# Optimization experiments

Measured on AMD Instinct MI355X. Metric: run time of the kernel, lower is better.

Reference implementation:

```python
import jax, jax.numpy as jnp
import numpy as np

N_NODES = 50000
N_EDGES = 1600000
IN_DIM = 128
OUT_DIM = 16
N_HEADS = 8


def setup_inputs() -> dict:
    key = jax.random.key(0)
    ks = jax.random.split(key, 9)
    s = 1.0 / np.sqrt(IN_DIM)
    return {
        "h": jax.random.normal(ks[0], (N_NODES, IN_DIM), jnp.float32),
        "Wq": jax.random.normal(ks[1], (IN_DIM, OUT_DIM * N_HEADS), jnp.float32) * s,
        "bq": jax.random.normal(ks[2], (OUT_DIM * N_HEADS,), jnp.float32) * 0.01,
        "Wk": jax.random.normal(ks[3], (IN_DIM, OUT_DIM * N_HEADS), jnp.float32) * s,
        "bk": jax.random.normal(ks[4], (OUT_DIM * N_HEADS,), jnp.float32) * 0.01,
        "Wv": jax.random.normal(ks[5], (IN_DIM, OUT_DIM * N_HEADS), jnp.float32) * s,
        "bv": jax.random.normal(ks[6], (OUT_DIM * N_HEADS,), jnp.float32) * 0.01,
        "src": jax.random.randint(ks[7], (N_EDGES,), 0, N_NODES, jnp.int32),
        "dst": jax.random.randint(ks[8], (N_EDGES,), 0, N_NODES, jnp.int32),
    }


def reference(h, Wq, bq, Wk, bk, Wv, bv, src, dst):
    n_nodes = h.shape[0]
    # node-wise Q/K/V projections -> [N, H, D]
    Q = (h @ Wq + bq).reshape(n_nodes, N_HEADS, OUT_DIM)
    K = (h @ Wk + bk).reshape(n_nodes, N_HEADS, OUT_DIM)
    V = (h @ Wv + bv).reshape(n_nodes, N_HEADS, OUT_DIM)
    # edge-wise score: (K[src] * Q[dst]).sum(-1), scaled-exp with clamp
    score = jnp.sum(K[src] * Q[dst], axis=-1)  # [E, H]
    score = jnp.exp(jnp.clip(score / np.sqrt(OUT_DIM), -5.0, 5.0))
    # scatter-sum weighted values and normalizers to dst nodes
    msg = V[src] * score[:, :, None]  # [E, H, D]
    wV = jax.ops.segment_sum(msg, dst, num_segments=n_nodes)  # [N, H, D]
    z = jax.ops.segment_sum(score, dst, num_segments=n_nodes)  # [N, H]
    return wV / (z[:, :, None] + 1e-6)
```

## Files before the change

### kernel.cpp

```cpp
#include <hip/hip_runtime.h>
#include <hip/hip_bf16.h>
#include <cstddef>

#define N_NODES 50000
#define N_EDGES 1600000
#define IN_DIM 128
#define OUT_DIM 16
#define N_HEADS 8
#define QKV_DIM 128
#define HS_STRIDE 136
#define OS_STRIDE 392

#define SUBB 3125
#define BCAP 1024
#define BH_CHUNK 8192
#define BH_BLOCKS 196
#define GEMM_BLOCKS 782
#define FUSED_BLOCKS (BH_BLOCKS + GEMM_BLOCKS)

typedef __hip_bfloat16 bf16;
typedef short bf16x8 __attribute__((ext_vector_type(8)));
typedef float f32x4  __attribute__((ext_vector_type(4)));

__device__ __forceinline__ float b2f(bf16 x) { return __bfloat162float(x); }

__device__ __forceinline__ float u16tof(unsigned int u) {
    unsigned int x = u << 16;
    float f;
    __builtin_memcpy(&f, &x, 4);
    return f;
}

__device__ __forceinline__ unsigned short f2bf(float v) {
    bf16 b = __float2bfloat16(v);
    unsigned short u;
    __builtin_memcpy(&u, &b, 2);
    return u;
}

__global__ __launch_bounds__(256) void sentinel_kernel(unsigned short* __restrict__ out, int n) {
    int i = blockIdx.x * 256 + threadIdx.x;
    if (i < n) out[i] = 0x42C8;
}

__global__ __launch_bounds__(256) void prep_kernel(
    const unsigned short* __restrict__ hraw,
    const void* __restrict__ Wqr, const void* __restrict__ bqr,
    const void* __restrict__ Wkr, const void* __restrict__ bkr,
    const void* __restrict__ Wvr, const void* __restrict__ bvr,
    int* __restrict__ flag,
    unsigned short* __restrict__ Wfrag, float* __restrict__ bias_f)
{
    __shared__ int red[256];
    const int t   = threadIdx.x;
    const int tid = blockIdx.x * 256 + t;

    int cnt = 0;
    for (int i = t; i < 8192; i += 256) {
        unsigned short u = hraw[i];
        int e = (u >> 7) & 0xFF;
        if (e == 0xFF || e > 0x85 || (e == 0 && (u & 0x7F) != 0)) cnt++;
    }
    red[t] = cnt;
    __syncthreads();
    for (int s = 128; s > 0; s >>= 1) {
        if (t < s) red[t] += red[t + s];
        __syncthreads();
    }
    const bool f32 = (red[0] > 100);
    if (blockIdx.x == 0 && t == 0) *flag = red[0];

    if (tid < 384) {
        int mat = tid >> 7, c = tid & 127;
        const void* bp = (mat == 0) ? bqr : (mat == 1) ? bkr : bvr;
        bias_f[tid] = f32 ? ((const float*)bp)[c] : b2f(((const bf16*)bp)[c]);
    }

    int l  = tid & 63;
    int s  = (tid >> 6) & 3;
    int nt = tid >> 8;
    int n  = nt * 16 + (l & 15);
    int k0 = s * 32 + (l >> 4) * 8;
    int mat = n >> 7, c = n & 127;
    const void* Wp = (mat == 0) ? Wqr : (mat == 1) ? Wkr : Wvr;

    unsigned short v[8];
#pragma unroll
    for (int j = 0; j < 8; ++j) {
        int k = k0 + j;
        float w = f32 ? ((const float*)Wp)[k * QKV_DIM + c]
                      : b2f(((const bf16*)Wp)[k * QKV_DIM + c]);
        v[j] = f2bf(w);
    }
    ushort4* o = (ushort4*)(Wfrag + (size_t)tid * 8);
    o[0] = make_ushort4(v[0], v[1], v[2], v[3]);
    o[1] = make_ushort4(v[4], v[5], v[6], v[7]);
}

__global__ __launch_bounds__(256) void fused_gs_kernel(
    const void* __restrict__ hraw,
    const unsigned short* __restrict__ Wfrag, const float* __restrict__ bias_f,
    const int* __restrict__ flag,
    unsigned short* __restrict__ Qt, unsigned short* __restrict__ KVt,
    const int* __restrict__ src, const int* __restrict__ dst,
    unsigned int* __restrict__ packed, unsigned int* __restrict__ offcnt)
{
    __shared__ __align__(16) unsigned char arena[64 * OS_STRIDE * 2];
    const int t = threadIdx.x;

    if (blockIdx.x < BH_BLOCKS) {
        int* lcnt           = (int*)arena;
        unsigned int* stage = (unsigned int*)(arena + 12544);
        int* sm             = (int*)(arena + 45312);
        int* carryp         = (int*)(arena + 46336);

        const int b    = blockIdx.x;
        const int base = b * BH_CHUNK;
        const int nb   = min(N_EDGES - base, BH_CHUNK);

        for (int i = t; i < SUBB; i += 256) lcnt[i] = 0;
        if (t == 0) *carryp = 0;
        __syncthreads();

        for (int i = t; i < nb; i += 256)
            atomicAdd(&lcnt[dst[base + i] >> 4], 1);
        __syncthreads();

        for (int c = 0; c < 13; ++c) {
            int i = c * 256 + t;
            int x = (i < SUBB) ? lcnt[i] : 0;
            int v = x;
            sm[t] = v;
            __syncthreads();
            for (int s = 1; s < 256; s <<= 1) {
                int a = (t >= s) ? sm[t - s] : 0;
                __syncthreads();
                v += a;
                sm[t] = v;
                __syncthreads();
            }
            int off = *carryp + v - x;
            if (i < SUBB) {
                offcnt[(size_t)b * SUBB + i] =
                    ((unsigned int)off << 16) | (unsigned int)x;
                lcnt[i] = off;
            }
            __syncthreads();
            if (t == 255) *carryp += v;
            __syncthreads();
        }

        for (int i = t; i < nb; i += 256) {
            int d = dst[base + i];
            int bk = d >> 4;
            int pos = atomicAdd(&lcnt[bk], 1);
            stage[pos] = (unsigned int)src[base + i] | ((unsigned int)(d & 15) << 16);
        }
        __syncthreads();

        for (int i = t; i < nb; i += 256)
            packed[base + i] = stage[i];

    } else {
        unsigned short* smem = (unsigned short*)arena;

        const bool f32 = (*flag > 100);
        const int m0 = (blockIdx.x - BH_BLOCKS) * 64;

#pragma unroll
        for (int it = 0; it < 8; ++it) {
            int idx = it * 1024 + t * 4;
            int r = idx >> 7, k = idx & 127;
            int row = m0 + r;
            ushort4 w4 = make_ushort4(0, 0, 0, 0);
            if (row < N_NODES) {
                if (f32) {
                    float4 v4 = ((const float4*)hraw)[(size_t)row * 32 + (k >> 2)];
                    w4 = make_ushort4(f2bf(v4.x), f2bf(v4.y), f2bf(v4.z), f2bf(v4.w));
                } else {
                    uint2 u = ((const uint2*)hraw)[(size_t)row * 32 + (k >> 2)];
                    w4 = make_ushort4((unsigned short)(u.x & 0xffffu), (unsigned short)(u.x >> 16),
                                      (unsigned short)(u.y & 0xffffu), (unsigned short)(u.y >> 16));
                }
            }
            *(ushort4*)&smem[r * HS_STRIDE + k] = w4;
        }
        __syncthreads();

        const int lane = t & 63;
        const int wave = t >> 6;
        const int qd   = lane >> 4;
        const int ln15 = lane & 15;

        bf16x8 afr[4][4];
#pragma unroll
        for (int ms = 0; ms < 4; ++ms)
#pragma unroll
            for (int s = 0; s < 4; ++s)
                afr[ms][s] = *(const bf16x8*)&smem[(ms * 16 + ln15) * HS_STRIDE + s * 32 + qd * 8];

        __syncthreads();

#pragma unroll
        for (int i = 0; i < 6; ++i) {
            const int nt  = wave + i * 4;
            const int col = nt * 16 + ln15;
            const float bs = bias_f[col];
            const int mat = col >> 7, c127 = col & 127;
            const int ocol = (mat == 0) ? c127
                           : 128 + 8 * (c127 >> 2) + (c127 & 3) + ((mat == 2) ? 4 : 0);

            bf16x8 bfr[4];
#pragma unroll
            for (int s = 0; s < 4; ++s)
                bfr[s] = *(const bf16x8*)(Wfrag + ((size_t)(nt * 4 + s) * 64 + lane) * 8);

#pragma unroll
            for (int ms = 0; ms < 4; ++ms) {
                f32x4 acc = {0.f, 0.f, 0.f, 0.f};
#pragma unroll
                for (int s = 0; s < 4; ++s)
                    acc = __builtin_amdgcn_mfma_f32_16x16x32_bf16(afr[ms][s], bfr[s], acc, 0, 0, 0);
#pragma unroll
                for (int r = 0; r < 4; ++r) {
                    int rl = ms * 16 + qd * 4 + r;
                    smem[rl * OS_STRIDE + ocol] = f2bf(acc[r] + bs);
                }
            }
        }
        __syncthreads();

        for (int q = t; q < 1024; q += 256) {
            int row = q >> 4, c = q & 15;
            int grow = m0 + row;
            if (grow < N_NODES)
                ((uint4*)Qt)[grow * 16 + c] = *(const uint4*)&smem[row * OS_STRIDE + c * 8];
        }
        for (int q = t; q < 2048; q += 256) {
            int row = q >> 5, g = q & 31;
            int grow = m0 + row;
            if (grow < N_NODES)
                ((uint4*)KVt)[grow * 32 + g] = *(const uint4*)&smem[row * OS_STRIDE + 128 + g * 8];
        }
    }
}

__global__ __launch_bounds__(256) void bucket_agg_kernel(
    const unsigned short* __restrict__ Qt, const unsigned short* __restrict__ KVt,
    const unsigned int* __restrict__ packed, const unsigned int* __restrict__ offcnt,
    const int* __restrict__ flag, void* __restrict__ out)
{
    __shared__ unsigned int   lds_pk[BCAP];
    __shared__ unsigned short lds_src[BCAP];
    __shared__ int runoff[BH_BLOCKS], runcnt[BH_BLOCKS], runpfx[BH_BLOCKS];
    __shared__ int cnt16[16], base16[16], cur16[16];
    __shared__ int nb_s;

    const int sb = blockIdx.x;
    const int t  = threadIdx.x;

    if (t < 16) { cnt16[t] = 0; cur16[t] = 0; }
    if (t < BH_BLOCKS) {
        unsigned int oc = offcnt[(size_t)t * SUBB + sb];
        runoff[t] = t * BH_CHUNK + (int)(oc >> 16);
        runcnt[t] = (int)(oc & 0xffffu);
    }
    __syncthreads();

    {
        int* sm = (int*)lds_pk;
        int x = (t < BH_BLOCKS) ? runcnt[t] : 0;
        int v = x;
        sm[t] = v;
        __syncthreads();
        for (int s = 1; s < 256; s <<= 1) {
            int a = (t >= s) ? sm[t - s] : 0;
            __syncthreads();
            v += a;
            sm[t] = v;
            __syncthreads();
        }
        if (t < BH_BLOCKS) runpfx[t] = v - x;
        if (t == 255) nb_s = v;
        __syncthreads();
    }
    const int nb = min(nb_s, BCAP);

    for (int r = t; r < BH_BLOCKS; r += 256) {
        int ro = runoff[r], rc = runcnt[r], rp = runpfx[r];
        for (int j = 0; j < rc; ++j) {
            int dpos = rp + j;
            if (dpos < BCAP) {
                unsigned int pk = packed[ro + j];
                lds_pk[dpos] = pk;
                atomicAdd(&cnt16[(pk >> 16) & 15], 1);
            }
        }
    }
    __syncthreads();
    if (t == 0) {
        int acc = 0;
#pragma unroll
        for (int i = 0; i < 16; ++i) { base16[i] = acc; acc += cnt16[i]; }
    }
    __syncthreads();
    for (int j = t; j < nb; j += 256) {
        unsigned int pk = lds_pk[j];
        int dl = (pk >> 16) & 15;
        int pos = base16[dl] + atomicAdd(&cur16[dl], 1);
        lds_src[pos] = (unsigned short)(pk & 0xffffu);
    }
    __syncthreads();

    const int wave = t >> 6;
    const int lane = t & 63;
    const int half = lane >> 5;
    const int hl   = lane & 31;
    const uint4* KV4 = (const uint4*)KVt;
    const bool of32 = (*flag > 100);

    for (int dl = wave; dl < 16; dl += 4) {
        const int d = sb * 16 + dl;
        uint2 qw = ((const uint2*)Qt)[d * 32 + hl];
        const float q0 = u16tof(qw.x & 0xffffu), q1 = u16tof(qw.x >> 16);
        const float q2 = u16tof(qw.y & 0xffffu), q3 = u16tof(qw.y >> 16);
        const int off = base16[dl];
        const int n   = cnt16[dl];

        float a0 = 0.f, a1 = 0.f, a2 = 0.f, a3 = 0.f, zz = 0.f;

#define CONSUME(KV, SCMASK)                                                     \
        {                                                                       \
            float p = fmaf(u16tof((KV).x & 0xffffu), q0,                        \
                      fmaf(u16tof((KV).x >> 16), q1,                            \
                      fmaf(u16tof((KV).y & 0xffffu), q2,                        \
                           u16tof((KV).y >> 16) * q3)));                        \
            p += __shfl_xor(p, 1);                                              \
            p += __shfl_xor(p, 2);                                              \
            float sc = __expf(__builtin_amdgcn_fmed3f(p * 0.25f, -5.f, 5.f));   \
            sc *= (SCMASK);                                                     \
            a0 = fmaf(u16tof((KV).z & 0xffffu), sc, a0);                        \
            a1 = fmaf(u16tof((KV).z >> 16),     sc, a1);                        \
            a2 = fmaf(u16tof((KV).w & 0xffffu), sc, a2);                        \
            a3 = fmaf(u16tof((KV).w >> 16),     sc, a3);                        \
            zz += sc;                                                           \
        }

        int j = 0;
        for (; j + 8 <= n; j += 8) {
            int e[4];
#pragma unroll
            for (int u = 0; u < 4; ++u) e[u] = lds_src[off + j + 2 * u + half];
            uint4 kv[4];
#pragma unroll
            for (int u = 0; u < 4; ++u) kv[u] = KV4[e[u] * 32 + hl];
#pragma unroll
            for (int u = 0; u < 4; ++u) CONSUME(kv[u], 1.f)
        }
        for (; j + 2 <= n; j += 2) {
            int e = lds_src[off + j + half];
            uint4 kv = KV4[e * 32 + hl];
            CONSUME(kv, 1.f)
        }
        if (j < n) {
            int e = lds_src[off + j];
            uint4 kv = KV4[e * 32 + hl];
            CONSUME(kv, (half == 0) ? 1.f : 0.f)
        }
#undef CONSUME

        a0 += __shfl_xor(a0, 32);
        a1 += __shfl_xor(a1, 32);
        a2 += __shfl_xor(a2, 32);
        a3 += __shfl_xor(a3, 32);
        zz += __shfl_xor(zz, 32);

        const float inv = 1.f / (zz + 1e-6f);
        const float r0 = a0 * inv, r1 = a1 * inv, r2 = a2 * inv, r3 = a3 * inv;

        if (half == 0) {
            if (of32) {
                ((float4*)out)[d * 32 + hl] = make_float4(r0, r1, r2, r3);
            } else {
                unsigned int w0 = ((unsigned int)f2bf(r1) << 16) | f2bf(r0);
                unsigned int w1 = ((unsigned int)f2bf(r3) << 16) | f2bf(r2);
                ((uint2*)out)[d * 32 + hl] = make_uint2(w0, w1);
            }
        }
    }
}

extern "C" void kernel_launch(void* const* d_in, const int* in_sizes, int n_in,
                              void* d_out, int out_size, void* d_ws, size_t ws_size,
                              hipStream_t stream)
{
    const void* h  = d_in[0];
    const void* Wq = d_in[1];
    const void* bq = d_in[2];
    const void* Wk = d_in[3];
    const void* bk = d_in[4];
    const void* Wv = d_in[5];
    const void* bv = d_in[6];
    const int*  src = (const int*)d_in[7];
    const int*  dst = (const int*)d_in[8];

    const size_t NQ = (size_t)N_NODES * QKV_DIM;
    const size_t WFRAG_N = 24 * 4 * 64 * 8;
    const size_t PACKED_N = (size_t)BH_BLOCKS * BH_CHUNK;
    const size_t OFFCNT_N = (size_t)BH_BLOCKS * SUBB;

    const size_t need = 3 * NQ * 2 + WFRAG_N * 2 + 384 * 4 + 64
                      + PACKED_N * 4 + OFFCNT_N * 4;

    if (ws_size < need) {
        sentinel_kernel<<<(out_size + 255) / 256, 256, 0, stream>>>((unsigned short*)d_out, out_size);
        return;
    }

    unsigned short* Qt  = (unsigned short*)d_ws;
    unsigned short* KVt = Qt + NQ;
    unsigned short* Wfrag = KVt + 2 * NQ;
    float* bias_f = (float*)(Wfrag + WFRAG_N);
    int* flag     = (int*)(bias_f + 384);
    unsigned int* packed = (unsigned int*)(flag + 16);
    unsigned int* offcnt = packed + PACKED_N;

    prep_kernel<<<24, 256, 0, stream>>>((const unsigned short*)h,
        Wq, bq, Wk, bk, Wv, bv, flag, Wfrag, bias_f);

    fused_gs_kernel<<<FUSED_BLOCKS, 256, 0, stream>>>(h, Wfrag, bias_f, flag,
        Qt, KVt, src, dst, packed, offcnt);

    bucket_agg_kernel<<<SUBB, 256, 0, stream>>>(Qt, KVt, packed, offcnt, flag, d_out);
}
```

Before: 256.1 us.

## Scatter edges into fixed-capacity global buckets and shrink GEMM tile to 32 rows

Replaces the per-block prefix-scan and offset/count table with global per-bucket atomic cursors, so edges are written directly into fixed-capacity (768) slots per 16-node bucket. The aggregation kernel then reads one contiguous run per bucket instead of gathering 196 runs. The GEMM part now uses 32-row tiles with a smaller LDS arena and writes Q, K and V in three passes, which should raise occupancy. The risk is that bucket slots are silently truncated when a bucket holds more than GCAP edges, and the atomic cursor ordering is nondeterministic.

```diff
diff --git a/kernel.cpp b/kernel.cpp
--- a/kernel.cpp
+++ b/kernel.cpp
@@ -9,13 +9,13 @@
 #define N_HEADS 8
 #define QKV_DIM 128
 #define HS_STRIDE 136
-#define OS_STRIDE 392
 
 #define SUBB 3125
-#define BCAP 1024
+#define GCAP 768
 #define BH_CHUNK 8192
 #define BH_BLOCKS 196
-#define GEMM_BLOCKS 782
+#define GEMM_M 32
+#define GEMM_BLOCKS 1563
 #define FUSED_BLOCKS (BH_BLOCKS + GEMM_BLOCKS)
 
 typedef __hip_bfloat16 bf16;
@@ -49,11 +49,14 @@
     const void* __restrict__ Wkr, const void* __restrict__ bkr,
     const void* __restrict__ Wvr, const void* __restrict__ bvr,
     int* __restrict__ flag,
-    unsigned short* __restrict__ Wfrag, float* __restrict__ bias_f)
+    unsigned short* __restrict__ Wfrag, float* __restrict__ bias_f,
+    int* __restrict__ gcur)
 {
     __shared__ int red[256];
     const int t   = threadIdx.x;
     const int tid = blockIdx.x * 256 + t;
+
+    for (int i = tid; i < SUBB; i += 24 * 256) gcur[i] = 0;
 
     int cnt = 0;
     for (int i = t; i < 8192; i += 256) {
@@ -103,72 +106,47 @@
     const int* __restrict__ flag,
     unsigned short* __restrict__ Qt, unsigned short* __restrict__ KVt,
     const int* __restrict__ src, const int* __restrict__ dst,
-    unsigned int* __restrict__ packed, unsigned int* __restrict__ offcnt)
+    unsigned int* __restrict__ gpacked, int* __restrict__ gcur)
 {
-    __shared__ __align__(16) unsigned char arena[64 * OS_STRIDE * 2];
+    __shared__ __align__(16) unsigned char arena[12544];
     const int t = threadIdx.x;
 
     if (blockIdx.x < BH_BLOCKS) {
-        int* lcnt           = (int*)arena;
-        unsigned int* stage = (unsigned int*)(arena + 12544);
-        int* sm             = (int*)(arena + 45312);
-        int* carryp         = (int*)(arena + 46336);
+        int* lcnt = (int*)arena;
 
         const int b    = blockIdx.x;
         const int base = b * BH_CHUNK;
         const int nb   = min(N_EDGES - base, BH_CHUNK);
 
         for (int i = t; i < SUBB; i += 256) lcnt[i] = 0;
-        if (t == 0) *carryp = 0;
         __syncthreads();
 
         for (int i = t; i < nb; i += 256)
             atomicAdd(&lcnt[dst[base + i] >> 4], 1);
         __syncthreads();
 
-        for (int c = 0; c < 13; ++c) {
-            int i = c * 256 + t;
-            int x = (i < SUBB) ? lcnt[i] : 0;
-            int v = x;
-            sm[t] = v;
-            __syncthreads();
-            for (int s = 1; s < 256; s <<= 1) {
-                int a = (t >= s) ? sm[t - s] : 0;
-                __syncthreads();
-                v += a;
-                sm[t] = v;
-                __syncthreads();
-            }
-            int off = *carryp + v - x;
-            if (i < SUBB) {
-                offcnt[(size_t)b * SUBB + i] =
-                    ((unsigned int)off << 16) | (unsigned int)x;
-                lcnt[i] = off;
-            }
-            __syncthreads();
-            if (t == 255) *carryp += v;
-            __syncthreads();
-        }
+        for (int i = t; i < SUBB; i += 256) {
+            int c = lcnt[i];
+            if (c) lcnt[i] = i * GCAP + atomicAdd(&gcur[i], c);
+        }
+        __syncthreads();
 
         for (int i = t; i < nb; i += 256) {
-            int d = dst[base + i];
+            int d  = dst[base + i];
             int bk = d >> 4;
             int pos = atomicAdd(&lcnt[bk], 1);
-            stage[pos] = (unsigned int)src[base + i] | ((unsigned int)(d & 15) << 16);
-        }
-        __syncthreads();
-
-        for (int i = t; i < nb; i += 256)
-            packed[base + i] = stage[i];
+            if (pos < (bk + 1) * GCAP)
+                gpacked[pos] = (unsigned int)src[base + i] | ((unsigned int)(d & 15) << 16);
+        }
 
     } else {
         unsigned short* smem = (unsigned short*)arena;
 
         const bool f32 = (*flag > 100);
-        const int m0 = (blockIdx.x - BH_BLOCKS) * 64;
-
-#pragma unroll
-        for (int it = 0; it < 8; ++it) {
+        const int m0 = (blockIdx.x - BH_BLOCKS) * GEMM_M;
+
+#pragma unroll
+        for (int it = 0; it < 4; ++it) {
             int idx = it * 1024 + t * 4;
             int r = idx >> 7, k = idx & 127;
             int row = m0 + r;
@@ -192,9 +170,9 @@
         const int qd   = lane >> 4;
         const int ln15 = lane & 15;
 
-        bf16x8 afr[4][4];
-#pragma unroll
-        for (int ms = 0; ms < 4; ++ms)
+        bf16x8 afr[2][4];
+#pragma unroll
+        for (int ms = 0; ms < 2; ++ms)
 #pragma unroll
             for (int s = 0; s < 4; ++s)
                 afr[ms][s] = *(const bf16x8*)&smem[(ms * 16 + ln15) * HS_STRIDE + s * 32 + qd * 8];
@@ -202,100 +180,78 @@
         __syncthreads();
 
 #pragma unroll
-        for (int i = 0; i < 6; ++i) {
-            const int nt  = wave + i * 4;
-            const int col = nt * 16 + ln15;
-            const float bs = bias_f[col];
-            const int mat = col >> 7, c127 = col & 127;
-            const int ocol = (mat == 0) ? c127
-                           : 128 + 8 * (c127 >> 2) + (c127 & 3) + ((mat == 2) ? 4 : 0);
-
-            bf16x8 bfr[4];
-#pragma unroll
-            for (int s = 0; s < 4; ++s)
-                bfr[s] = *(const bf16x8*)(Wfrag + ((size_t)(nt * 4 + s) * 64 + lane) * 8);
-
-#pragma unroll
-            for (int ms = 0; ms < 4; ++ms) {
-                f32x4 acc = {0.f, 0.f, 0.f, 0.f};
+        for (int p = 0; p < 3; ++p) {
+#pragma unroll
+            for (int ii = 0; ii < 2; ++ii) {
+                const int i   = 2 * p + ii;
+                const int nt  = wave + i * 4;
+                const int col = nt * 16 + ln15;
+                const float bs = bias_f[col];
+                const int c127 = col & 127;
+
+                bf16x8 bfr[4];
 #pragma unroll
                 for (int s = 0; s < 4; ++s)
-                    acc = __builtin_amdgcn_mfma_f32_16x16x32_bf16(afr[ms][s], bfr[s], acc, 0, 0, 0);
-#pragma unroll
-                for (int r = 0; r < 4; ++r) {
-                    int rl = ms * 16 + qd * 4 + r;
-                    smem[rl * OS_STRIDE + ocol] = f2bf(acc[r] + bs);
+                    bfr[s] = *(const bf16x8*)(Wfrag + ((size_t)(nt * 4 + s) * 64 + lane) * 8);
+
+#pragma unroll
+                for (int ms = 0; ms < 2; ++ms) {
+                    f32x4 acc = {0.f, 0.f, 0.f, 0.f};
+#pragma unroll
+                    for (int s = 0; s < 4; ++s)
+                        acc = __builtin_amdgcn_mfma_f32_16x16x32_bf16(afr[ms][s], bfr[s], acc, 0, 0, 0);
+#pragma unroll
+                    for (int r = 0; r < 4; ++r) {
+                        int rl = ms * 16 + qd * 4 + r;
+                        smem[rl * HS_STRIDE + c127] = f2bf(acc[r] + bs);
+                    }
                 }
             }
-        }
-        __syncthreads();
-
-        for (int q = t; q < 1024; q += 256) {
-            int row = q >> 4, c = q & 15;
-            int grow = m0 + row;
-            if (grow < N_NODES)
-                ((uint4*)Qt)[grow * 16 + c] = *(const uint4*)&smem[row * OS_STRIDE + c * 8];
-        }
-        for (int q = t; q < 2048; q += 256) {
-            int row = q >> 5, g = q & 31;
-            int grow = m0 + row;
-            if (grow < N_NODES)
-                ((uint4*)KVt)[grow * 32 + g] = *(const uint4*)&smem[row * OS_STRIDE + 128 + g * 8];
+            __syncthreads();
+            if (p == 0) {
+                for (int q = t; q < 512; q += 256) {
+                    int row = q >> 4, c = q & 15;
+                    int grow = m0 + row;
+                    if (grow < N_NODES)
+                        ((uint4*)Qt)[grow * 16 + c] = *(const uint4*)&smem[row * HS_STRIDE + c * 8];
+                }
+            } else {
+                for (int q = t; q < 1024; q += 256) {
+                    int row = q >> 5, g = q & 31;
+                    int grow = m0 + row;
+                    if (grow < N_NODES)
+                        ((uint2*)KVt)[(size_t)grow * 64 + g * 2 + (p - 1)] =
+                            *(const uint2*)&smem[row * HS_STRIDE + g * 4];
+                }
+            }
+            __syncthreads();
         }
     }
 }
 
 __global__ __launch_bounds__(256) void bucket_agg_kernel(
     const unsigned short* __restrict__ Qt, const unsigned short* __restrict__ KVt,
-    const unsigned int* __restrict__ packed, const unsigned int* __restrict__ offcnt,
+    const unsigned int* __restrict__ gpacked, const int* __restrict__ gcur,
     const int* __restrict__ flag, void* __restrict__ out)
 {
-    __shared__ unsigned int   lds_pk[BCAP];
-    __shared__ unsigned short lds_src[BCAP];
-    __shared__ int runoff[BH_BLOCKS], runcnt[BH_BLOCKS], runpfx[BH_BLOCKS];
+    __shared__ unsigned int   lds_pk[GCAP];
+    __shared__ unsigned short lds_src[GCAP];
     __shared__ int cnt16[16], base16[16], cur16[16];
-    __shared__ int nb_s;
+    __shared__ int n_s;
 
     const int sb = blockIdx.x;
     const int t  = threadIdx.x;
 
     if (t < 16) { cnt16[t] = 0; cur16[t] = 0; }
-    if (t < BH_BLOCKS) {
-        unsigned int oc = offcnt[(size_t)t * SUBB + sb];
-        runoff[t] = t * BH_CHUNK + (int)(oc >> 16);
-        runcnt[t] = (int)(oc & 0xffffu);
-    }
-    __syncthreads();
-
-    {
-        int* sm = (int*)lds_pk;
-        int x = (t < BH_BLOCKS) ? runcnt[t] : 0;
-        int v = x;
-        sm[t] = v;
-        __syncthreads();
-        for (int s = 1; s < 256; s <<= 1) {
-            int a = (t >= s) ? sm[t - s] : 0;
-            __syncthreads();
-            v += a;
-            sm[t] = v;
-            __syncthreads();
-        }
-        if (t < BH_BLOCKS) runpfx[t] = v - x;
-        if (t == 255) nb_s = v;
-        __syncthreads();
-    }
-    const int nb = min(nb_s, BCAP);
-
-    for (int r = t; r < BH_BLOCKS; r += 256) {
-        int ro = runoff[r], rc = runcnt[r], rp = runpfx[r];
-        for (int j = 0; j < rc; ++j) {
-            int dpos = rp + j;
-            if (dpos < BCAP) {
-                unsigned int pk = packed[ro + j];
-                lds_pk[dpos] = pk;
-                atomicAdd(&cnt16[(pk >> 16) & 15], 1);
-            }
-        }
+    if (t == 0) n_s = min(gcur[sb], GCAP);
+    __syncthreads();
+    const int n  = n_s;
+    const int gb = sb * GCAP;
+
+    for (int j = t; j < n; j += 256) {
+        unsigned int pk = gpacked[gb + j];
+        lds_pk[j] = pk;
+        atomicAdd(&cnt16[(pk >> 16) & 15], 1);
     }
     __syncthreads();
     if (t == 0) {
@@ -304,7 +260,7 @@
         for (int i = 0; i < 16; ++i) { base16[i] = acc; acc += cnt16[i]; }
     }
     __syncthreads();
-    for (int j = t; j < nb; j += 256) {
+    for (int j = t; j < n; j += 256) {
         unsigned int pk = lds_pk[j];
         int dl = (pk >> 16) & 15;
         int pos = base16[dl] + atomicAdd(&cur16[dl], 1);
@@ -325,7 +281,7 @@
         const float q0 = u16tof(qw.x & 0xffffu), q1 = u16tof(qw.x >> 16);
         const float q2 = u16tof(qw.y & 0xffffu), q3 = u16tof(qw.y >> 16);
         const int off = base16[dl];
-        const int n   = cnt16[dl];
+        const int nd  = cnt16[dl];
 
         float a0 = 0.f, a1 = 0.f, a2 = 0.f, a3 = 0.f, zz = 0.f;
 
@@ -347,7 +303,7 @@
         }
 
         int j = 0;
-        for (; j + 8 <= n; j += 8) {
+        for (; j + 8 <= nd; j += 8) {
             int e[4];
 #pragma unroll
             for (int u = 0; u < 4; ++u) e[u] = lds_src[off + j + 2 * u + half];
@@ -357,12 +313,12 @@
 #pragma unroll
             for (int u = 0; u < 4; ++u) CONSUME(kv[u], 1.f)
         }
-        for (; j + 2 <= n; j += 2) {
+        for (; j + 2 <= nd; j += 2) {
             int e = lds_src[off + j + half];
             uint4 kv = KV4[e * 32 + hl];
             CONSUME(kv, 1.f)
         }
-        if (j < n) {
+        if (j < nd) {
             int e = lds_src[off + j];
             uint4 kv = KV4[e * 32 + hl];
             CONSUME(kv, (half == 0) ? 1.f : 0.f)
@@ -406,11 +362,10 @@
 
     const size_t NQ = (size_t)N_NODES * QKV_DIM;
     const size_t WFRAG_N = 24 * 4 * 64 * 8;
-    const size_t PACKED_N = (size_t)BH_BLOCKS * BH_CHUNK;
-    const size_t OFFCNT_N = (size_t)BH_BLOCKS * SUBB;
+    const size_t GPACK_N = (size_t)SUBB * GCAP;
 
     const size_t need = 3 * NQ * 2 + WFRAG_N * 2 + 384 * 4 + 64
-                      + PACKED_N * 4 + OFFCNT_N * 4;
+                      + (size_t)SUBB * 4 + 64 + GPACK_N * 4;
 
     if (ws_size < need) {
         sentinel_kernel<<<(out_size + 255) / 256, 256, 0, stream>>>((unsigned short*)d_out, out_size);
@@ -422,14 +377,14 @@
     unsigned short* Wfrag = KVt + 2 * NQ;
     float* bias_f = (float*)(Wfrag + WFRAG_N);
     int* flag     = (int*)(bias_f + 384);
-    unsigned int* packed = (unsigned int*)(flag + 16);
-    unsigned int* offcnt = packed + PACKED_N;
+    int* gcur     = flag + 16;
+    unsigned int* gpacked = (unsigned int*)(gcur + SUBB + 11);
 
     prep_kernel<<<24, 256, 0, stream>>>((const unsigned short*)h,
-        Wq, bq, Wk, bk, Wv, bv, flag, Wfrag, bias_f);
+        Wq, bq, Wk, bk, Wv, bv, flag, Wfrag, bias_f, gcur);
 
     fused_gs_kernel<<<FUSED_BLOCKS, 256, 0, stream>>>(h, Wfrag, bias_f, flag,
-        Qt, KVt, src, dst, packed, offcnt);
-
-    bucket_agg_kernel<<<SUBB, 256, 0, stream>>>(Qt, KVt, packed, offcnt, flag, d_out);
-}
+        Qt, KVt, src, dst, gpacked, gcur);
+
+    bucket_agg_kernel<<<SUBB, 256, 0, stream>>>(Qt, KVt, gpacked, gcur, flag, d_out);
+}
```

After: 269.5 us. 1.05x slower.
